# Performance work log

Measured on AMD Instinct MI355X. Metric: run time of the kernel, lower is better.

## Reference

```python
import jax, jax.numpy as jnp
import numpy as np

N_BITS = 32
HIDDEN = 128


def _neighborhoods(z):
    """z: (B,k,H,W) -> (B,k,9,H,W) 3x3 neighborhoods (zero-padded), center zeroed.

    Position ordering matches F.unfold(kernel_size=3): row-major over (di,dj),
    so index 4 is the center, which the module masks to 0.
    """
    B, k, H, W = z.shape
    zp = jnp.pad(z, ((0, 0), (0, 0), (1, 1), (1, 1)))
    views = []
    for di in range(3):
        for dj in range(3):
            if di == 1 and dj == 1:  # center masked out
                views.append(jnp.zeros_like(z))
            else:
                views.append(zp[:, :, di:di + H, dj:dj + W])
    return jnp.stack(views, axis=2)  # (B,k,9,H,W)


def setup_inputs() -> dict:
    key = jax.random.key(0)
    k1, k2, k3, k4, k5 = jax.random.split(key, 5)
    B, k, H, W = 8, N_BITS, 256, 256
    z = jax.random.normal(k1, (B, k, H, W), dtype=jnp.float32)
    # nn.Linear(9*k, hidden): weight (hidden, 9k), feature order = k-outer, 9-inner
    W1 = jax.random.normal(k2, (HIDDEN, 9 * k), dtype=jnp.float32) * (1.0 / np.sqrt(9 * k))
    b1 = jax.random.normal(k3, (HIDDEN,), dtype=jnp.float32) * 0.01
    W2 = jax.random.normal(k4, (k, HIDDEN), dtype=jnp.float32) * (1.0 / np.sqrt(HIDDEN))
    b2 = jax.random.normal(k5, (k,), dtype=jnp.float32) * 0.01
    return {"z": z, "W1": W1, "b1": b1, "W2": W2, "b2": b2}


def reference(z, W1, b1, W2, b2):
    B, k, H, W = z.shape
    win = _neighborhoods(z)                      # (B,k,9,H,W)
    W1r = W1.reshape(HIDDEN, k, 9)               # split (9k) -> (k,9), k-outer
    h = jnp.einsum('bkphw,dkp->bdhw', win, W1r) + b1[None, :, None, None]
    h = jax.nn.relu(h)
    logits = jnp.einsum('bdhw,kd->bkhw', h, W2) + b2[None, :, None, None]
    return logits  # (B,k,H,W)
```

## Files before the change

kernel.cpp:

```cpp
#include <hip/hip_runtime.h>


#define KC 32
#define HH 256
#define WW 256
#define HID 128
#define YS 8
#define ZROW 2640
#define HSTR 132

typedef __attribute__((ext_vector_type(8))) short short8;
typedef __attribute__((ext_vector_type(4))) float f32x4;

#define BARRIER() asm volatile("s_waitcnt lgkmcnt(0)\n\ts_barrier" ::: "memory")
#define SCHED_FENCE() asm volatile("" ::: "memory")

__device__ __forceinline__ unsigned short f2bf(float f) {
    union { float f; unsigned int i; } x; x.f = f;
    unsigned int r = x.i + 0x7FFFu + ((x.i >> 16) & 1u);
    return (unsigned short)(r >> 16);
}

__device__ __forceinline__ short8 pack8(const float* v) {
    union { short8 s; unsigned int u[4]; } w;
    union { float f; unsigned int i; } uu[8];
#pragma unroll
    for (int j = 0; j < 8; ++j) uu[j].f = v[j];
#pragma unroll
    for (int k = 0; k < 4; ++k)
        w.u[k] = __builtin_amdgcn_perm(uu[2 * k + 1].i, uu[2 * k].i, 0x07060302u);
    return w.s;
}

__global__ void prep_weights(const float* __restrict__ w1,
                             const float* __restrict__ w2,
                             unsigned short* __restrict__ w1t,
                             unsigned short* __restrict__ w2t) {
    int i = blockIdx.x * 256 + threadIdx.x;
    if (i < 9 * HID * KC) {
        int c = i & 31;
        int d = (i >> 5) & 127;
        int p = i >> 12;
        w1t[i] = f2bf(w1[d * (9 * KC) + c * 9 + p]);
    } else if (i < 9 * HID * KC + KC * HID) {
        int j = i - 9 * HID * KC;
        w2t[j] = f2bf(w2[j]);
    }
}

__global__ __launch_bounds__(256, 4) void local_pred_kernel(
    const float* __restrict__ zg,
    const unsigned short* __restrict__ w1t,
    const float* __restrict__ b1g,
    const unsigned short* __restrict__ w2t,
    const float* __restrict__ b2g,
    float* __restrict__ outg)
{
    __shared__ __attribute__((aligned(16))) unsigned short z_lds[4 * ZROW];
    __shared__ __attribute__((aligned(16))) unsigned short h_lds[64 * HSTR];
    __shared__ __attribute__((aligned(16))) unsigned short halo_lds[7 * 2 * 32];

    const int tid  = threadIdx.x;
    const int bidx = blockIdx.x;
    const int x0 = (bidx & 3) << 6;
    const int y0 = ((bidx >> 2) & 31) * YS;
    const int b  = bidx >> 7;

    const int l = tid & 63;
    const int o = tid >> 6;

    const int wave = tid >> 6;
    const int lane = tid & 63;
    const int lr = lane & 15;
    const int lq = lane >> 4;

    const float* zb = zg + (size_t)b * KC * HH * WW;

#pragma unroll
    for (int dy = 0; dy < 3; ++dy) {
        const int gy = y0 - 1 + dy;
        const bool ok = (unsigned)gy < (unsigned)HH;
        const int gyc = ok ? gy : 0;
        const float* p = zb + ((size_t)(o * 8) * HH + gyc) * WW + x0 + l;
        float t8[8];
#pragma unroll
        for (int j = 0; j < 8; ++j) t8[j] = ok ? p[(size_t)j * HH * WW] : 0.f;
        *(short8*)&z_lds[(dy * 66 + l + 1) * 40 + o * 8] = pack8(t8);
        SCHED_FENCE();
    }
    {
        const int s = tid & 1, oc = (tid >> 1) & 3, dy = tid >> 3;
        const int gy = y0 - 1 + dy;
        const int gx = x0 - 1 + s * 65;
        const bool ok = (tid < 24) && ((unsigned)gy < (unsigned)HH) &&
                        ((unsigned)gx < (unsigned)WW);
        const float* q = zb + ((size_t)(oc * 8) * HH + (ok ? gy : 0)) * WW + (ok ? gx : 0);
        float t8[8];
#pragma unroll
        for (int j = 0; j < 8; ++j) t8[j] = ok ? q[(size_t)j * HH * WW] : 0.f;
        if (tid < 24)
            *(short8*)&z_lds[(dy * 66 + s * 65) * 40 + oc * 8] = pack8(t8);
        SCHED_FENCE();
    }
    {
        const int fi = tid - 64;
        const int s = fi & 1, oc = (fi >> 1) & 3, fr = fi >> 3;
        const int gy = y0 + 2 + fr;
        const int gx = x0 - 1 + s * 65;
        const bool ok = (tid >= 64) && (tid < 120) && (gy < HH) &&
                        ((unsigned)gx < (unsigned)WW);
        const float* q = zb + ((size_t)(oc * 8) * HH + (ok ? gy : 0)) * WW + (ok ? gx : 0);
        float t8[8];
#pragma unroll
        for (int j = 0; j < 8; ++j) t8[j] = ok ? q[(size_t)j * HH * WW] : 0.f;
        if (tid >= 64 && tid < 120)
            *(short8*)&halo_lds[(fr * 2 + s) * 32 + oc * 8] = pack8(t8);
        SCHED_FENCE();
    }

    float bias1[2], bias2[2];
#pragma unroll
    for (int nt = 0; nt < 2; ++nt) bias1[nt] = b1g[wave * 32 + nt * 16 + lr];
#pragma unroll
    for (int nt = 0; nt < 2; ++nt) bias2[nt] = b2g[nt * 16 + lr];

    BARRIER();

    const int tap_di[8] = {0, 0, 0, 1, 1, 2, 2, 2};
    const int tap_dj[8] = {0, 1, 2, 0, 2, 0, 1, 2};

    float mv8[8];

#pragma unroll
    for (int r = 0; r < YS; ++r) {
        const int y = y0 + r;
        const int S0 = r & 3, S1 = (r + 1) & 3, S2 = (r + 2) & 3, S3 = (r + 3) & 3;

        if (r < 7) {
            const int gy = y + 2;
            const bool ok = gy < HH;
            const float* p = zb + ((size_t)(o * 8) * HH + (ok ? gy : 0)) * WW + x0 + l;
#pragma unroll
            for (int j = 0; j < 8; ++j) mv8[j] = ok ? p[(size_t)j * HH * WW] : 0.f;
        }
        SCHED_FENCE();

        f32x4 acc[4][2];
#pragma unroll
        for (int mt = 0; mt < 4; ++mt)
#pragma unroll
            for (int nt = 0; nt < 2; ++nt)
                acc[mt][nt] = (f32x4){0.f, 0.f, 0.f, 0.f};

        const int rowoff[3] = {S0 * ZROW, S1 * ZROW, S2 * ZROW};
#pragma unroll
        for (int t = 0; t < 8; ++t) {
            const int di = tap_di[t], dj = tap_dj[t];
            const int p = di * 3 + dj;
            short8 afr[4];
#pragma unroll
            for (int mt = 0; mt < 4; ++mt)
                afr[mt] = *(const short8*)&z_lds[rowoff[di] + (mt * 16 + lr + dj) * 40 + lq * 8];
            short8 bfr[2];
#pragma unroll
            for (int nt = 0; nt < 2; ++nt)
                bfr[nt] = *(const short8*)&w1t[p * (HID * KC) + (wave * 32 + nt * 16 + lr) * KC + lq * 8];
#pragma unroll
            for (int nt = 0; nt < 2; ++nt)
#pragma unroll
                for (int mt = 0; mt < 4; ++mt)
                    acc[mt][nt] = __builtin_amdgcn_mfma_f32_16x16x32_bf16(
                        afr[mt], bfr[nt], acc[mt][nt], 0, 0, 0);
        }

#pragma unroll
        for (int nt = 0; nt < 2; ++nt) {
            const int d = wave * 32 + nt * 16 + lr;
#pragma unroll
            for (int mt = 0; mt < 4; ++mt)
#pragma unroll
                for (int rr = 0; rr < 4; ++rr) {
                    float v = acc[mt][nt][rr] + bias1[nt];
                    v = v > 0.f ? v : 0.f;
                    const int m = mt * 16 + lq * 4 + rr;
                    h_lds[m * HSTR + d] = f2bf(v);
                }
        }
        BARRIER();

        f32x4 acc2[2];
        acc2[0] = (f32x4){0.f, 0.f, 0.f, 0.f};
        acc2[1] = (f32x4){0.f, 0.f, 0.f, 0.f};
        const int m2 = wave * 16 + lr;
#pragma unroll
        for (int k4 = 0; k4 < 4; ++k4) {
            short8 afr = *(const short8*)&h_lds[m2 * HSTR + k4 * 32 + lq * 8];
#pragma unroll
            for (int nt = 0; nt < 2; ++nt) {
                short8 bfr = *(const short8*)&w2t[(nt * 16 + lr) * HID + k4 * 32 + lq * 8];
                acc2[nt] = __builtin_amdgcn_mfma_f32_16x16x32_bf16(afr, bfr, acc2[nt], 0, 0, 0);
            }
        }

#pragma unroll
        for (int nt = 0; nt < 2; ++nt) {
            const int kout = nt * 16 + lr;
            f32x4 pk;
#pragma unroll
            for (int rr = 0; rr < 4; ++rr) pk[rr] = acc2[nt][rr] + bias2[nt];
            const int mb = wave * 16 + lq * 4;
            const size_t off = ((size_t)(b * KC + kout) * HH + y) * WW + x0 + mb;
            *(f32x4*)&outg[off] = pk;
        }

        if (r < 7) {
            *(short8*)&z_lds[(S3 * 66 + l + 1) * 40 + o * 8] = pack8(mv8);
            if (tid < 8) {
                const int side = tid & 1, oct = tid >> 1;
                short8 hv = *(const short8*)&halo_lds[(r * 2 + side) * 32 + oct * 8];
                *(short8*)&z_lds[(S3 * 66 + side * 65) * 40 + oct * 8] = hv;
            }
        }
        BARRIER();
    }
}

extern "C" void kernel_launch(void* const* d_in, const int* in_sizes, int n_in,
                              void* d_out, int out_size, void* d_ws, size_t ws_size,
                              hipStream_t stream)
{
    const float* z  = (const float*)d_in[0];
    const float* W1 = (const float*)d_in[1];
    const float* b1 = (const float*)d_in[2];
    const float* W2 = (const float*)d_in[3];
    const float* b2 = (const float*)d_in[4];
    float* out = (float*)d_out;
    unsigned short* w1t = (unsigned short*)d_ws;
    unsigned short* w2t = (unsigned short*)d_ws + 9 * HID * KC;

    hipLaunchKernelGGL(prep_weights, dim3(160), dim3(256), 0, stream, W1, W2, w1t, w2t);
    hipLaunchKernelGGL(local_pred_kernel, dim3(8 * 4 * (HH / YS)), dim3(256), 0, stream,
                       z, w1t, b1, w2t, b2, out);
}
```

Measured before the change: 177.9 us.

## Split first GEMM by pixel rows per wave to drop mid-row block barrier

Each wave now computes all 128 hidden units for its own 16 pixels (instead of 32 hidden units for all 64 pixels), swapping MFMA operands so the hidden dimension lands in the accumulator rows. Because each wave then writes and reads only its own rows of the hidden scratch buffer, the block-wide barrier between the two GEMMs is removed and packed 32-bit stores replace scalar bf16 stores. The trade-off is that each wave loads all eight W1 fragments per tap from global memory (more weight traffic, fewer z reads), and the hidden-row stride is changed to reduce LDS bank conflicts.

After: 381.7 us. 2.14x slower.

```diff
diff --git a/kernel.cpp b/kernel.cpp
--- a/kernel.cpp
+++ b/kernel.cpp
@@ -7,7 +7,7 @@
 #define HID 128
 #define YS 8
 #define ZROW 2640
-#define HSTR 132
+#define HSTR 136
 
 typedef __attribute__((ext_vector_type(8))) short short8;
 typedef __attribute__((ext_vector_type(4))) float f32x4;
@@ -57,7 +57,7 @@
     float* __restrict__ outg)
 {
     __shared__ __attribute__((aligned(16))) unsigned short z_lds[4 * ZROW];
-    __shared__ __attribute__((aligned(16))) unsigned short h_lds[64 * HSTR];
+    __shared__ __attribute__((aligned(16))) unsigned short h_scr[64 * HSTR];
     __shared__ __attribute__((aligned(16))) unsigned short halo_lds[7 * 2 * 32];
 
     const int tid  = threadIdx.x;
@@ -118,9 +118,7 @@
         SCHED_FENCE();
     }
 
-    float bias1[2], bias2[2];
-#pragma unroll
-    for (int nt = 0; nt < 2; ++nt) bias1[nt] = b1g[wave * 32 + nt * 16 + lr];
+    float bias2[2];
 #pragma unroll
     for (int nt = 0; nt < 2; ++nt) bias2[nt] = b2g[nt * 16 + lr];
 
@@ -130,6 +128,8 @@
     const int tap_dj[8] = {0, 1, 2, 0, 2, 0, 1, 2};
 
     float mv8[8];
+
+    const int hbase = (wave * 16 + lr) * HSTR;
 
 #pragma unroll
     for (int r = 0; r < YS; ++r) {
@@ -145,59 +145,47 @@
         }
         SCHED_FENCE();
 
-        f32x4 acc[4][2];
-#pragma unroll
-        for (int mt = 0; mt < 4; ++mt)
-#pragma unroll
-            for (int nt = 0; nt < 2; ++nt)
-                acc[mt][nt] = (f32x4){0.f, 0.f, 0.f, 0.f};
+        f32x4 acc[8];
+#pragma unroll
+        for (int nt = 0; nt < 8; ++nt)
+            acc[nt] = (f32x4){0.f, 0.f, 0.f, 0.f};
 
         const int rowoff[3] = {S0 * ZROW, S1 * ZROW, S2 * ZROW};
 #pragma unroll
         for (int t = 0; t < 8; ++t) {
             const int di = tap_di[t], dj = tap_dj[t];
             const int p = di * 3 + dj;
-            short8 afr[4];
-#pragma unroll
-            for (int mt = 0; mt < 4; ++mt)
-                afr[mt] = *(const short8*)&z_lds[rowoff[di] + (mt * 16 + lr + dj) * 40 + lq * 8];
-            short8 bfr[2];
-#pragma unroll
-            for (int nt = 0; nt < 2; ++nt)
-                bfr[nt] = *(const short8*)&w1t[p * (HID * KC) + (wave * 32 + nt * 16 + lr) * KC + lq * 8];
-#pragma unroll
-            for (int nt = 0; nt < 2; ++nt)
-#pragma unroll
-                for (int mt = 0; mt < 4; ++mt)
-                    acc[mt][nt] = __builtin_amdgcn_mfma_f32_16x16x32_bf16(
-                        afr[mt], bfr[nt], acc[mt][nt], 0, 0, 0);
-        }
-
-#pragma unroll
-        for (int nt = 0; nt < 2; ++nt) {
-            const int d = wave * 32 + nt * 16 + lr;
-#pragma unroll
-            for (int mt = 0; mt < 4; ++mt)
-#pragma unroll
-                for (int rr = 0; rr < 4; ++rr) {
-                    float v = acc[mt][nt][rr] + bias1[nt];
-                    v = v > 0.f ? v : 0.f;
-                    const int m = mt * 16 + lq * 4 + rr;
-                    h_lds[m * HSTR + d] = f2bf(v);
-                }
-        }
-        BARRIER();
+            short8 zfr = *(const short8*)&z_lds[rowoff[di] + (wave * 16 + lr + dj) * 40 + lq * 8];
+#pragma unroll
+            for (int nt = 0; nt < 8; ++nt) {
+                short8 wfr = *(const short8*)&w1t[p * (HID * KC) + (nt * 16 + lr) * KC + lq * 8];
+                acc[nt] = __builtin_amdgcn_mfma_f32_16x16x32_bf16(wfr, zfr, acc[nt], 0, 0, 0);
+            }
+        }
+
+#pragma unroll
+        for (int nt = 0; nt < 8; ++nt) {
+            const f32x4 bv = *(const f32x4*)&b1g[nt * 16 + lq * 4];
+#pragma unroll
+            for (int e = 0; e < 2; ++e) {
+                float v0 = acc[nt][2 * e]     + bv[2 * e];
+                float v1 = acc[nt][2 * e + 1] + bv[2 * e + 1];
+                v0 = v0 > 0.f ? v0 : 0.f;
+                v1 = v1 > 0.f ? v1 : 0.f;
+                unsigned int pk = ((unsigned int)f2bf(v1) << 16) | f2bf(v0);
+                *(unsigned int*)&h_scr[hbase + nt * 16 + lq * 4 + 2 * e] = pk;
+            }
+        }
 
         f32x4 acc2[2];
         acc2[0] = (f32x4){0.f, 0.f, 0.f, 0.f};
         acc2[1] = (f32x4){0.f, 0.f, 0.f, 0.f};
-        const int m2 = wave * 16 + lr;
-#pragma unroll
-        for (int k4 = 0; k4 < 4; ++k4) {
-            short8 afr = *(const short8*)&h_lds[m2 * HSTR + k4 * 32 + lq * 8];
+#pragma unroll
+        for (int kk = 0; kk < 4; ++kk) {
+            short8 afr = *(const short8*)&h_scr[hbase + kk * 32 + lq * 8];
 #pragma unroll
             for (int nt = 0; nt < 2; ++nt) {
-                short8 bfr = *(const short8*)&w2t[(nt * 16 + lr) * HID + k4 * 32 + lq * 8];
+                short8 bfr = *(const short8*)&w2t[(nt * 16 + lr) * HID + kk * 32 + lq * 8];
                 acc2[nt] = __builtin_amdgcn_mfma_f32_16x16x32_bf16(afr, bfr, acc2[nt], 0, 0, 0);
             }
         }
```
